# Kernel tuning notes

Measured on AMD Instinct MI355X. Metric: run time of the kernel, lower is better.

The kernel has to match this reference:

```python
import jax, jax.numpy as jnp
import numpy as np

TOP_K = 2


def setup_inputs() -> dict:
    key = jax.random.key(0)
    k0, k1, k2, k3, k4 = jax.random.split(key, 5)
    B, S, H, F, E = 2, 1024, 2048, 7168, 8
    scale = 0.02
    return {
        "hidden_states": jax.random.normal(k0, (B, S, H), jnp.float32),
        "Wg": jax.random.normal(k1, (E, H), jnp.float32) * scale,
        "w1": jax.random.normal(k2, (E, F, H), jnp.float32) * scale,
        "w3": jax.random.normal(k3, (E, F, H), jnp.float32) * scale,
        "w2": jax.random.normal(k4, (E, H, F), jnp.float32) * scale,
    }


def reference(hidden_states, Wg, w1, w3, w2):
    B, S, H = hidden_states.shape
    E = Wg.shape[0]
    x = hidden_states.reshape(-1, H)                      # [T, H]
    T = x.shape[0]

    # Router: logits -> softmax (float32) -> top-k -> renormalize
    router_logits = jnp.einsum("th,eh->te", x, Wg)        # [T, E]
    probs = jax.nn.softmax(router_logits.astype(jnp.float32), axis=-1)
    top_w, top_idx = jax.lax.top_k(probs, TOP_K)          # [T, K]
    top_w = top_w / jnp.sum(top_w, axis=-1, keepdims=True)
    top_w = top_w.astype(x.dtype)

    # Combine weights: [T, E], zero for unselected experts
    combine = jnp.zeros((T, E), x.dtype).at[
        jnp.arange(T)[:, None], top_idx
    ].add(top_w)

    out = jnp.zeros((T, H), x.dtype)
    for e in range(E):
        h = jax.nn.silu(x @ w1[e].T) * (x @ w3[e].T)      # [T, F]
        out = out + (h @ w2[e].T) * combine[:, e:e + 1]   # [T, H]

    return out.reshape(B, S, H), router_logits
```

## Files before the change

### kernel.cpp

```cpp
#include <hip/hip_runtime.h>

#define T_TOK 2048
#define H_DIM 2048
#define F_DIM 7168
#define E_NUM 8
#define MAX_SLOTS 5120
#define BM 128
#define BN 128
#define BK 64

typedef __attribute__((ext_vector_type(8))) _Float16 f16x8;
typedef __attribute__((ext_vector_type(4))) _Float16 f16x4;
typedef __attribute__((ext_vector_type(4))) float    f32x4;

#define GLL(g, l) __builtin_amdgcn_global_load_lds(                          \
    (const __attribute__((address_space(1))) void*)(g),                      \
    (__attribute__((address_space(3))) void*)(l), 16, 0, 0)


__global__ __launch_bounds__(256) void cvtw_kernel(const float* __restrict__ src,
                                                   _Float16* __restrict__ dst) {
    size_t i = ((size_t)blockIdx.x * 256 + threadIdx.x) * 8;
    float4 a = *(const float4*)(src + i);
    float4 b = *(const float4*)(src + i + 4);
    f16x8 h;
    h[0]=(_Float16)a.x; h[1]=(_Float16)a.y; h[2]=(_Float16)a.z; h[3]=(_Float16)a.w;
    h[4]=(_Float16)b.x; h[5]=(_Float16)b.y; h[6]=(_Float16)b.z; h[7]=(_Float16)b.w;
    *(f16x8*)(dst + i) = h;
}

__global__ __launch_bounds__(256) void router_kernel(
    const float* __restrict__ x, const float* __restrict__ wg,
    float* __restrict__ logits_out, int* __restrict__ tk_e,
    float* __restrict__ tk_w, int* __restrict__ meta) {
    int wave = threadIdx.x >> 6;
    int lane = threadIdx.x & 63;
    int t = blockIdx.x * 4 + wave;
    const float* xr = x + (size_t)t * H_DIM;

    float xv[32];
#pragma unroll
    for (int i = 0; i < 8; i++) {
        float4 v = *(const float4*)(xr + i * 256 + lane * 4);
        xv[i*4+0] = v.x; xv[i*4+1] = v.y; xv[i*4+2] = v.z; xv[i*4+3] = v.w;
    }
    float lg[E_NUM];
#pragma unroll
    for (int e = 0; e < E_NUM; e++) {
        const float* wr = wg + (size_t)e * H_DIM;
        float acc = 0.f;
#pragma unroll
        for (int i = 0; i < 8; i++) {
            float4 v = *(const float4*)(wr + i * 256 + lane * 4);
            acc += xv[i*4+0]*v.x + xv[i*4+1]*v.y + xv[i*4+2]*v.z + xv[i*4+3]*v.w;
        }
#pragma unroll
        for (int s = 32; s > 0; s >>= 1) acc += __shfl_xor(acc, s, 64);
        lg[e] = acc;
    }
    if (lane == 0) {
        float b0 = -3e38f, b1 = -3e38f; int i0 = 0, i1 = 0;
#pragma unroll
        for (int e = 0; e < E_NUM; e++) {
            float le = lg[e];
            if (le > b0)      { b1 = b0; i1 = i0; b0 = le; i0 = e; }
            else if (le > b1) { b1 = le; i1 = e; }
        }
        float w0 = 1.f / (1.f + __expf(b1 - b0));
        float w1v = 1.f - w0;
#pragma unroll
        for (int e = 0; e < E_NUM; e++) logits_out[(size_t)t * E_NUM + e] = lg[e];
        tk_e[t*2+0] = i0; tk_w[t*2+0] = w0;
        tk_e[t*2+1] = i1; tk_w[t*2+1] = w1v;
        atomicAdd(&meta[i0], 1);
        atomicAdd(&meta[i1], 1);
    }
}

__global__ void scan_kernel(int* __restrict__ meta, int* __restrict__ slot_tok,
                            float* __restrict__ slot_w) {
    int lane = threadIdx.x;
    int cnts[E_NUM], pads[E_NUM], bases[E_NUM];
    int run = 0;
#pragma unroll
    for (int e = 0; e < E_NUM; e++) {
        cnts[e] = meta[e];
        pads[e] = (cnts[e] + BM - 1) & ~(BM - 1);
        bases[e] = run;
        run += pads[e];
    }
    if (lane < E_NUM) { meta[8 + lane] = pads[lane]; meta[16 + lane] = bases[lane]; }
    for (int e = 0; e < E_NUM; e++)
        for (int i = cnts[e] + lane; i < pads[e]; i += 64) {
            slot_tok[bases[e] + i] = 0;
            slot_w[bases[e] + i] = 0.f;
        }
}

__global__ __launch_bounds__(256) void assign_kernel(
    const int* __restrict__ tk_e, const float* __restrict__ tk_w,
    int* __restrict__ meta, int* __restrict__ slot_tok, float* __restrict__ slot_w) {
    int t = blockIdx.x * 256 + threadIdx.x;
    if (t >= T_TOK) return;
#pragma unroll
    for (int k = 0; k < 2; k++) {
        int e = tk_e[t*2+k];
        int pos = atomicAdd(&meta[24 + e], 1);
        int s = meta[16 + e] + pos;
        slot_tok[s] = t;
        slot_w[s] = tk_w[t*2+k];
    }
}


__global__ __launch_bounds__(256, 2) void ffn1_kernel(
    const _Float16* __restrict__ xb, const _Float16* __restrict__ w1h,
    const _Float16* __restrict__ w3h, const int* __restrict__ slot_tok,
    const int* __restrict__ meta, _Float16* __restrict__ hbuf) {
    int e = blockIdx.z;
    int cntpad = meta[8 + e];
    int mb = blockIdx.y;
    if (mb * BM >= cntpad) return;
    int base = meta[16 + e];
    int nb = blockIdx.x;

    __shared__ _Float16 sA[BM][BK];
    __shared__ _Float16 sB1[BN][BK];
    __shared__ _Float16 sB3[BN][BK];

    int tid = threadIdx.x;
    int lane = tid & 63;
    int wave = tid >> 6;
    int wm = wave >> 1, wn = wave & 1;
    int lr = lane & 15, lk = (lane >> 4) * 8;

    int rsub = lane >> 3;
    int colc = (lane & 7) * 8;
    int slot0 = base + mb * BM;

    const _Float16* aG[4];
    const _Float16* b1G[4];
    const _Float16* b3G[4];
#pragma unroll
    for (int q = 0; q < 4; q++) {
        int row = wave * 32 + q * 8 + rsub;
        int tok = slot_tok[slot0 + row];
        aG[q] = xb + (size_t)tok * H_DIM + colc;
        size_t wrow = (size_t)e * F_DIM + (size_t)nb * BN + row;
        b1G[q] = w1h + wrow * H_DIM + colc;
        b3G[q] = w3h + wrow * H_DIM + colc;
    }

    f32x4 zero = {0.f, 0.f, 0.f, 0.f};
    f32x4 acc1[4][4], acc3[4][4];
#pragma unroll
    for (int m = 0; m < 4; m++)
#pragma unroll
        for (int n = 0; n < 4; n++) { acc1[m][n] = zero; acc3[m][n] = zero; }

    for (int k0 = 0; k0 < H_DIM; k0 += BK) {
        __syncthreads();
#pragma unroll
        for (int q = 0; q < 4; q++) {
            GLL(aG[q] + k0,  &sA[wave * 32 + q * 8][0]);
            GLL(b1G[q] + k0, &sB1[wave * 32 + q * 8][0]);
            GLL(b3G[q] + k0, &sB3[wave * 32 + q * 8][0]);
        }
        __syncthreads();
#pragma unroll
        for (int ks = 0; ks < BK; ks += 32) {
            f16x8 af[4], bf1[4], bf3[4];
#pragma unroll
            for (int m = 0; m < 4; m++)
                af[m] = *(const f16x8*)(const void*)&sA[wm*64 + m*16 + lr][ks + lk];
#pragma unroll
            for (int n = 0; n < 4; n++) {
                bf1[n] = *(const f16x8*)(const void*)&sB1[wn*64 + n*16 + lr][ks + lk];
                bf3[n] = *(const f16x8*)(const void*)&sB3[wn*64 + n*16 + lr][ks + lk];
            }
#pragma unroll
            for (int m = 0; m < 4; m++)
#pragma unroll
                for (int n = 0; n < 4; n++) {
                    acc1[m][n] = __builtin_amdgcn_mfma_f32_16x16x32_f16(af[m], bf1[n], acc1[m][n], 0, 0, 0);
                    acc3[m][n] = __builtin_amdgcn_mfma_f32_16x16x32_f16(af[m], bf3[n], acc3[m][n], 0, 0, 0);
                }
        }
    }
    int row0 = mb * BM + wm * 64;
    int col0 = nb * BN + wn * 64;
#pragma unroll
    for (int m = 0; m < 4; m++) {
#pragma unroll
        for (int n = 0; n < 4; n++) {
            int col = col0 + n * 16 + lr;
            f32x4 v1 = acc1[m][n], v3 = acc3[m][n];
#pragma unroll
            for (int j = 0; j < 4; j++) {
                int slot = base + row0 + m * 16 + (lane >> 4) * 4 + j;
                float a1 = v1[j], a3 = v3[j];
                float hv = a1 * a3 / (1.f + __expf(-a1));
                hbuf[(size_t)slot * F_DIM + col] = (_Float16)hv;
            }
        }
    }
}

__global__ __launch_bounds__(256, 2) void ffn2_kernel(
    const _Float16* __restrict__ hbuf, const _Float16* __restrict__ w2h,
    const int* __restrict__ slot_tok, const float* __restrict__ slot_w,
    const int* __restrict__ meta, float* __restrict__ out) {
    int e = blockIdx.z;
    int cntpad = meta[8 + e];
    int mb = blockIdx.y;
    if (mb * BM >= cntpad) return;
    int base = meta[16 + e];
    int nb = blockIdx.x;

    __shared__ _Float16 sA[BM][BK];
    __shared__ _Float16 sB[BN][BK];

    int tid = threadIdx.x;
    int lane = tid & 63;
    int wave = tid >> 6;
    int wm = wave >> 1, wn = wave & 1;
    int lr = lane & 15, lk = (lane >> 4) * 8;

    int rsub = lane >> 3;
    int colc = (lane & 7) * 8;
    int slot0 = base + mb * BM;

    const _Float16* aG[4];
    const _Float16* bG[4];
#pragma unroll
    for (int q = 0; q < 4; q++) {
        int row = wave * 32 + q * 8 + rsub;
        aG[q] = hbuf + (size_t)(slot0 + row) * F_DIM + colc;
        bG[q] = w2h + ((size_t)e * H_DIM + (size_t)nb * BN + row) * F_DIM + colc;
    }

    f32x4 zero = {0.f, 0.f, 0.f, 0.f};
    f32x4 acc[4][4];
#pragma unroll
    for (int m = 0; m < 4; m++)
#pragma unroll
        for (int n = 0; n < 4; n++) acc[m][n] = zero;

    for (int k0 = 0; k0 < F_DIM; k0 += BK) {
        __syncthreads();
#pragma unroll
        for (int q = 0; q < 4; q++) {
            GLL(aG[q] + k0, &sA[wave * 32 + q * 8][0]);
            GLL(bG[q] + k0, &sB[wave * 32 + q * 8][0]);
        }
        __syncthreads();
#pragma unroll
        for (int ks = 0; ks < BK; ks += 32) {
            f16x8 af[4], bf[4];
#pragma unroll
            for (int m = 0; m < 4; m++)
                af[m] = *(const f16x8*)(const void*)&sA[wm*64 + m*16 + lr][ks + lk];
#pragma unroll
            for (int n = 0; n < 4; n++)
                bf[n] = *(const f16x8*)(const void*)&sB[wn*64 + n*16 + lr][ks + lk];
#pragma unroll
            for (int m = 0; m < 4; m++)
#pragma unroll
                for (int n = 0; n < 4; n++)
                    acc[m][n] = __builtin_amdgcn_mfma_f32_16x16x32_f16(af[m], bf[n], acc[m][n], 0, 0, 0);
        }
    }
    int row0 = mb * BM + wm * 64;
    int col0 = nb * BN + wn * 64;
#pragma unroll
    for (int m = 0; m < 4; m++) {
        int rb = row0 + m * 16 + (lane >> 4) * 4;
        int toks[4]; float wts[4];
#pragma unroll
        for (int j = 0; j < 4; j++) {
            int s = base + rb + j;
            toks[j] = slot_tok[s];
            wts[j]  = slot_w[s];
        }
#pragma unroll
        for (int n = 0; n < 4; n++) {
            int col = col0 + n * 16 + lr;
            f32x4 v = acc[m][n];
#pragma unroll
            for (int j = 0; j < 4; j++)
                atomicAdd(&out[(size_t)toks[j] * H_DIM + col], v[j] * wts[j]);
        }
    }
}

extern "C" void kernel_launch(void* const* d_in, const int* in_sizes, int n_in,
                              void* d_out, int out_size, void* d_ws, size_t ws_size,
                              hipStream_t stream) {
    const float* x  = (const float*)d_in[0];
    const float* wg = (const float*)d_in[1];
    const float* w1 = (const float*)d_in[2];
    const float* w3 = (const float*)d_in[3];
    const float* w2 = (const float*)d_in[4];
    float* out = (float*)d_out;
    float* logits = out + (size_t)T_TOK * H_DIM;

    const size_t WELEM = (size_t)E_NUM * F_DIM * H_DIM;

    char* ws = (char*)d_ws;
    _Float16* w1h  = (_Float16*)ws;
    _Float16* w3h  = w1h + WELEM;
    _Float16* w2h  = w3h + WELEM;
    _Float16* hbuf = w2h + WELEM;
    _Float16* xb   = hbuf + (size_t)MAX_SLOTS * F_DIM;
    char* p = (char*)(xb + (size_t)T_TOK * H_DIM);
    int*   slot_tok = (int*)p;   p += MAX_SLOTS * 4;
    float* slot_w   = (float*)p; p += MAX_SLOTS * 4;
    int*   tk_e     = (int*)p;   p += T_TOK * 2 * 4;
    float* tk_w     = (float*)p; p += T_TOK * 2 * 4;
    int*   meta     = (int*)p;

    hipMemsetAsync(d_out, 0, (size_t)out_size * sizeof(float), stream);
    hipMemsetAsync(meta, 0, 32 * sizeof(int), stream);

    cvtw_kernel<<<dim3(WELEM / (256 * 8)), 256, 0, stream>>>(w1, w1h);
    cvtw_kernel<<<dim3(WELEM / (256 * 8)), 256, 0, stream>>>(w3, w3h);
    cvtw_kernel<<<dim3(WELEM / (256 * 8)), 256, 0, stream>>>(w2, w2h);
    cvtw_kernel<<<dim3((size_t)T_TOK * H_DIM / (256 * 8)), 256, 0, stream>>>(x, xb);

    router_kernel<<<dim3(T_TOK / 4), 256, 0, stream>>>(x, wg, logits, tk_e, tk_w, meta);
    scan_kernel<<<dim3(1), 64, 0, stream>>>(meta, slot_tok, slot_w);
    assign_kernel<<<dim3(T_TOK / 256), 256, 0, stream>>>(tk_e, tk_w, meta, slot_tok, slot_w);

    ffn1_kernel<<<dim3(F_DIM / BN, 16, E_NUM), 256, 0, stream>>>(xb, w1h, w3h, slot_tok, meta, hbuf);
    ffn2_kernel<<<dim3(H_DIM / BN, 16, E_NUM), 256, 0, stream>>>(hbuf, w2h, slot_tok, slot_w, meta, out);
}
```

Before: 1.147 ms.

## Interleave w1/w3 weights, enlarge tiles, double-buffer LDS with swizzle in FFN kernels

Converts w1 and w3 into one interleaved fp16 buffer in 32-row blocks, so ffn1 runs a single 256x256 GEMM tile with 512 threads and applies the SiLU gate by pairing accumulator columns. Both FFN kernels now double-buffer LDS with global_load_lds prefetch two tiles ahead, use explicit vmcnt waits and raw barriers, and XOR-swizzle the LDS layout to avoid bank conflicts. ffn2 also moves to 128x256 tiles with 8 waves. The aim is to hide global load latency and raise MFMA utilisation. The cost is higher register and LDS pressure, with a possible occupancy risk from the larger tiles.

```diff
diff --git a/kernel.cpp b/kernel.cpp
--- a/kernel.cpp
+++ b/kernel.cpp
@@ -5,18 +5,33 @@
 #define F_DIM 7168
 #define E_NUM 8
 #define MAX_SLOTS 5120
-#define BM 128
-#define BN 128
-#define BK 64
+#define N13 (2 * F_DIM)
 
 typedef __attribute__((ext_vector_type(8))) _Float16 f16x8;
-typedef __attribute__((ext_vector_type(4))) _Float16 f16x4;
 typedef __attribute__((ext_vector_type(4))) float    f32x4;
 
 #define GLL(g, l) __builtin_amdgcn_global_load_lds(                          \
     (const __attribute__((address_space(1))) void*)(g),                      \
     (__attribute__((address_space(3))) void*)(l), 16, 0, 0)
 
+
+__global__ __launch_bounds__(256) void cvt13_kernel(const float* __restrict__ w1,
+                                                    const float* __restrict__ w3,
+                                                    _Float16* __restrict__ w13h) {
+    int b = blockIdx.x;
+    int e = b / N13;
+    int c = b - e * N13;
+    int blk = c >> 6, sub = c & 63;
+    int f = blk * 32 + (sub & 31);
+    const float* src = (sub < 32 ? w1 : w3) + ((size_t)e * F_DIM + f) * H_DIM + threadIdx.x * 8;
+    _Float16* dst = w13h + (size_t)b * H_DIM + threadIdx.x * 8;
+    float4 a = *(const float4*)src;
+    float4 bb = *(const float4*)(src + 4);
+    f16x8 h;
+    h[0]=(_Float16)a.x;  h[1]=(_Float16)a.y;  h[2]=(_Float16)a.z;  h[3]=(_Float16)a.w;
+    h[4]=(_Float16)bb.x; h[5]=(_Float16)bb.y; h[6]=(_Float16)bb.z; h[7]=(_Float16)bb.w;
+    *(f16x8*)dst = h;
+}
 
 __global__ __launch_bounds__(256) void cvtw_kernel(const float* __restrict__ src,
                                                    _Float16* __restrict__ dst) {
@@ -29,6 +44,7 @@
     *(f16x8*)(dst + i) = h;
 }
 
+
 __global__ __launch_bounds__(256) void router_kernel(
     const float* __restrict__ x, const float* __restrict__ wg,
     float* __restrict__ logits_out, int* __restrict__ tk_e,
@@ -85,7 +101,7 @@
 #pragma unroll
     for (int e = 0; e < E_NUM; e++) {
         cnts[e] = meta[e];
-        pads[e] = (cnts[e] + BM - 1) & ~(BM - 1);
+        pads[e] = (cnts[e] + 127) & ~127;
         bases[e] = run;
         run += pads[e];
     }
@@ -112,132 +128,160 @@
     }
 }
 
-
-__global__ __launch_bounds__(256, 2) void ffn1_kernel(
-    const _Float16* __restrict__ xb, const _Float16* __restrict__ w1h,
-    const _Float16* __restrict__ w3h, const int* __restrict__ slot_tok,
-    const int* __restrict__ meta, _Float16* __restrict__ hbuf) {
+__global__ __launch_bounds__(512, 2) void ffn1_kernel(
+    const _Float16* __restrict__ xb, const _Float16* __restrict__ w13h,
+    const int* __restrict__ slot_tok, const int* __restrict__ meta,
+    _Float16* __restrict__ hbuf) {
     int e = blockIdx.z;
     int cntpad = meta[8 + e];
     int mb = blockIdx.y;
-    if (mb * BM >= cntpad) return;
+    if (mb * 256 >= cntpad) return;
     int base = meta[16 + e];
     int nb = blockIdx.x;
 
-    __shared__ _Float16 sA[BM][BK];
-    __shared__ _Float16 sB1[BN][BK];
-    __shared__ _Float16 sB3[BN][BK];
-
-    int tid = threadIdx.x;
+    __shared__ _Float16 sA[2][256][64];
+    __shared__ _Float16 sB[2][256][64];
+
+    int tid  = threadIdx.x;
     int lane = tid & 63;
     int wave = tid >> 6;
-    int wm = wave >> 1, wn = wave & 1;
-    int lr = lane & 15, lk = (lane >> 4) * 8;
+    int wm = wave >> 2, wn = wave & 3;
+    int w8 = wave * 8;
+
+    int lr = lane & 15;
+    int sw = lane & 7;
+    int sg = lane >> 4;
+    int offk0 = lr * 64 + ((sg    ) ^ sw) * 8;
+    int offk1 = lr * 64 + ((sg + 4) ^ sw) * 8;
 
     int rsub = lane >> 3;
-    int colc = (lane & 7) * 8;
-    int slot0 = base + mb * BM;
+    int sl   = (lane & 7) ^ rsub;
+    int slot0 = base + mb * 256;
 
     const _Float16* aG[4];
-    const _Float16* b1G[4];
-    const _Float16* b3G[4];
+    const _Float16* bG[4];
 #pragma unroll
     for (int q = 0; q < 4; q++) {
-        int row = wave * 32 + q * 8 + rsub;
-        int tok = slot_tok[slot0 + row];
-        aG[q] = xb + (size_t)tok * H_DIM + colc;
-        size_t wrow = (size_t)e * F_DIM + (size_t)nb * BN + row;
-        b1G[q] = w1h + wrow * H_DIM + colc;
-        b3G[q] = w3h + wrow * H_DIM + colc;
+        int r = mb * 256 + q * 64 + w8 + rsub;
+        int tok = (r < cntpad) ? slot_tok[base + r] : 0;
+        aG[q] = xb + (size_t)tok * H_DIM + sl * 8;
+        bG[q] = w13h + ((size_t)e * N13 + (size_t)nb * 256 + q * 64 + w8 + rsub) * H_DIM + sl * 8;
     }
 
     f32x4 zero = {0.f, 0.f, 0.f, 0.f};
-    f32x4 acc1[4][4], acc3[4][4];
-#pragma unroll
-    for (int m = 0; m < 4; m++)
-#pragma unroll
-        for (int n = 0; n < 4; n++) { acc1[m][n] = zero; acc3[m][n] = zero; }
-
-    for (int k0 = 0; k0 < H_DIM; k0 += BK) {
-        __syncthreads();
-#pragma unroll
-        for (int q = 0; q < 4; q++) {
-            GLL(aG[q] + k0,  &sA[wave * 32 + q * 8][0]);
-            GLL(b1G[q] + k0, &sB1[wave * 32 + q * 8][0]);
-            GLL(b3G[q] + k0, &sB3[wave * 32 + q * 8][0]);
-        }
-        __syncthreads();
-#pragma unroll
-        for (int ks = 0; ks < BK; ks += 32) {
-            f16x8 af[4], bf1[4], bf3[4];
-#pragma unroll
-            for (int m = 0; m < 4; m++)
-                af[m] = *(const f16x8*)(const void*)&sA[wm*64 + m*16 + lr][ks + lk];
+    f32x4 acc[8][4];
+#pragma unroll
+    for (int m = 0; m < 8; m++)
+#pragma unroll
+        for (int n = 0; n < 4; n++) acc[m][n] = zero;
+
+    const int NT = H_DIM / 64;
+#pragma unroll
+    for (int q = 0; q < 4; q++) GLL(aG[q] + 0,  &sA[0][q*64 + w8][0]);
+#pragma unroll
+    for (int q = 0; q < 4; q++) GLL(bG[q] + 0,  &sB[0][q*64 + w8][0]);
+#pragma unroll
+    for (int q = 0; q < 4; q++) GLL(aG[q] + 64, &sA[1][q*64 + w8][0]);
+#pragma unroll
+    for (int q = 0; q < 4; q++) GLL(bG[q] + 64, &sB[1][q*64 + w8][0]);
+
+    for (int t = 0; t < NT; ++t) {
+        if (t < NT - 1) asm volatile("s_waitcnt vmcnt(8)" ::: "memory");
+        else            asm volatile("s_waitcnt vmcnt(0)" ::: "memory");
+        __builtin_amdgcn_sched_barrier(0);
+        __builtin_amdgcn_s_barrier();
+        __builtin_amdgcn_sched_barrier(0);
+        int bd = t & 1;
+        const _Float16* Ab = &sA[bd][wm * 128][0];
+        const _Float16* Bb = &sB[bd][wn * 64][0];
+        f16x8 bf[2][4];
+#pragma unroll
+        for (int n = 0; n < 4; n++) {
+            bf[0][n] = *(const f16x8*)(const void*)(Bb + n * 1024 + offk0);
+            bf[1][n] = *(const f16x8*)(const void*)(Bb + n * 1024 + offk1);
+        }
+        __builtin_amdgcn_s_setprio(1);
+#pragma unroll
+        for (int m = 0; m < 8; m++) {
+            f16x8 a0 = *(const f16x8*)(const void*)(Ab + m * 1024 + offk0);
+            f16x8 a1 = *(const f16x8*)(const void*)(Ab + m * 1024 + offk1);
 #pragma unroll
             for (int n = 0; n < 4; n++) {
-                bf1[n] = *(const f16x8*)(const void*)&sB1[wn*64 + n*16 + lr][ks + lk];
-                bf3[n] = *(const f16x8*)(const void*)&sB3[wn*64 + n*16 + lr][ks + lk];
+                acc[m][n] = __builtin_amdgcn_mfma_f32_16x16x32_f16(a0, bf[0][n], acc[m][n], 0, 0, 0);
+                acc[m][n] = __builtin_amdgcn_mfma_f32_16x16x32_f16(a1, bf[1][n], acc[m][n], 0, 0, 0);
             }
-#pragma unroll
-            for (int m = 0; m < 4; m++)
-#pragma unroll
-                for (int n = 0; n < 4; n++) {
-                    acc1[m][n] = __builtin_amdgcn_mfma_f32_16x16x32_f16(af[m], bf1[n], acc1[m][n], 0, 0, 0);
-                    acc3[m][n] = __builtin_amdgcn_mfma_f32_16x16x32_f16(af[m], bf3[n], acc3[m][n], 0, 0, 0);
+        }
+        __builtin_amdgcn_s_setprio(0);
+        __builtin_amdgcn_sched_barrier(0);
+        __builtin_amdgcn_s_barrier();
+        __builtin_amdgcn_sched_barrier(0);
+        if (t + 2 < NT) {
+            int k2 = (t + 2) * 64;
+#pragma unroll
+            for (int q = 0; q < 4; q++) GLL(aG[q] + k2, &sA[bd][q*64 + w8][0]);
+#pragma unroll
+            for (int q = 0; q < 4; q++) GLL(bG[q] + k2, &sB[bd][q*64 + w8][0]);
+        }
+    }
+
+    int row_e0 = mb * 256 + wm * 128;
+    int fb = nb * 128 + wn * 32;
+#pragma unroll
+    for (int m = 0; m < 8; m++) {
+#pragma unroll
+        for (int j = 0; j < 4; j++) {
+            int re = row_e0 + m * 16 + (lane >> 4) * 4 + j;
+            if (re < cntpad) {
+                size_t srow = (size_t)(base + re) * F_DIM;
+#pragma unroll
+                for (int n = 0; n < 2; n++) {
+                    float a1 = acc[m][n][j], a3 = acc[m][n + 2][j];
+                    float hv = a1 * a3 / (1.f + __expf(-a1));
+                    hbuf[srow + fb + n * 16 + lr] = (_Float16)hv;
                 }
-        }
-    }
-    int row0 = mb * BM + wm * 64;
-    int col0 = nb * BN + wn * 64;
-#pragma unroll
-    for (int m = 0; m < 4; m++) {
-#pragma unroll
-        for (int n = 0; n < 4; n++) {
-            int col = col0 + n * 16 + lr;
-            f32x4 v1 = acc1[m][n], v3 = acc3[m][n];
-#pragma unroll
-            for (int j = 0; j < 4; j++) {
-                int slot = base + row0 + m * 16 + (lane >> 4) * 4 + j;
-                float a1 = v1[j], a3 = v3[j];
-                float hv = a1 * a3 / (1.f + __expf(-a1));
-                hbuf[(size_t)slot * F_DIM + col] = (_Float16)hv;
             }
         }
     }
 }
 
-__global__ __launch_bounds__(256, 2) void ffn2_kernel(
+__global__ __launch_bounds__(512, 2) void ffn2_kernel(
     const _Float16* __restrict__ hbuf, const _Float16* __restrict__ w2h,
     const int* __restrict__ slot_tok, const float* __restrict__ slot_w,
     const int* __restrict__ meta, float* __restrict__ out) {
     int e = blockIdx.z;
     int cntpad = meta[8 + e];
     int mb = blockIdx.y;
-    if (mb * BM >= cntpad) return;
+    if (mb * 128 >= cntpad) return;
     int base = meta[16 + e];
     int nb = blockIdx.x;
 
-    __shared__ _Float16 sA[BM][BK];
-    __shared__ _Float16 sB[BN][BK];
-
-    int tid = threadIdx.x;
+    __shared__ _Float16 sA[2][128][64];
+    __shared__ _Float16 sB[2][256][64];
+
+    int tid  = threadIdx.x;
     int lane = tid & 63;
     int wave = tid >> 6;
-    int wm = wave >> 1, wn = wave & 1;
-    int lr = lane & 15, lk = (lane >> 4) * 8;
+    int wm = wave >> 2, wn = wave & 3;
+    int w8 = wave * 8;
+
+    int lr = lane & 15;
+    int sw = lane & 7;
+    int sg = lane >> 4;
+    int offk0 = lr * 64 + ((sg    ) ^ sw) * 8;
+    int offk1 = lr * 64 + ((sg + 4) ^ sw) * 8;
 
     int rsub = lane >> 3;
-    int colc = (lane & 7) * 8;
-    int slot0 = base + mb * BM;
-
-    const _Float16* aG[4];
+    int sl   = (lane & 7) ^ rsub;
+    int slot0 = base + mb * 128;
+
+    const _Float16* aG[2];
     const _Float16* bG[4];
 #pragma unroll
-    for (int q = 0; q < 4; q++) {
-        int row = wave * 32 + q * 8 + rsub;
-        aG[q] = hbuf + (size_t)(slot0 + row) * F_DIM + colc;
-        bG[q] = w2h + ((size_t)e * H_DIM + (size_t)nb * BN + row) * F_DIM + colc;
-    }
+    for (int q = 0; q < 2; q++)
+        aG[q] = hbuf + (size_t)(slot0 + q * 64 + w8 + rsub) * F_DIM + sl * 8;
+#pragma unroll
+    for (int q = 0; q < 4; q++)
+        bG[q] = w2h + ((size_t)e * H_DIM + (size_t)nb * 256 + q * 64 + w8 + rsub) * F_DIM + sl * 8;
 
     f32x4 zero = {0.f, 0.f, 0.f, 0.f};
     f32x4 acc[4][4];
@@ -246,32 +290,57 @@
 #pragma unroll
         for (int n = 0; n < 4; n++) acc[m][n] = zero;
 
-    for (int k0 = 0; k0 < F_DIM; k0 += BK) {
-        __syncthreads();
-#pragma unroll
-        for (int q = 0; q < 4; q++) {
-            GLL(aG[q] + k0, &sA[wave * 32 + q * 8][0]);
-            GLL(bG[q] + k0, &sB[wave * 32 + q * 8][0]);
-        }
-        __syncthreads();
-#pragma unroll
-        for (int ks = 0; ks < BK; ks += 32) {
-            f16x8 af[4], bf[4];
-#pragma unroll
-            for (int m = 0; m < 4; m++)
-                af[m] = *(const f16x8*)(const void*)&sA[wm*64 + m*16 + lr][ks + lk];
-#pragma unroll
-            for (int n = 0; n < 4; n++)
-                bf[n] = *(const f16x8*)(const void*)&sB[wn*64 + n*16 + lr][ks + lk];
-#pragma unroll
-            for (int m = 0; m < 4; m++)
-#pragma unroll
-                for (int n = 0; n < 4; n++)
-                    acc[m][n] = __builtin_amdgcn_mfma_f32_16x16x32_f16(af[m], bf[n], acc[m][n], 0, 0, 0);
-        }
-    }
-    int row0 = mb * BM + wm * 64;
-    int col0 = nb * BN + wn * 64;
+    const int NT = F_DIM / 64;
+#pragma unroll
+    for (int q = 0; q < 2; q++) GLL(aG[q] + 0,  &sA[0][q*64 + w8][0]);
+#pragma unroll
+    for (int q = 0; q < 4; q++) GLL(bG[q] + 0,  &sB[0][q*64 + w8][0]);
+#pragma unroll
+    for (int q = 0; q < 2; q++) GLL(aG[q] + 64, &sA[1][q*64 + w8][0]);
+#pragma unroll
+    for (int q = 0; q < 4; q++) GLL(bG[q] + 64, &sB[1][q*64 + w8][0]);
+
+    for (int t = 0; t < NT; ++t) {
+        if (t < NT - 1) asm volatile("s_waitcnt vmcnt(6)" ::: "memory");
+        else            asm volatile("s_waitcnt vmcnt(0)" ::: "memory");
+        __builtin_amdgcn_sched_barrier(0);
+        __builtin_amdgcn_s_barrier();
+        __builtin_amdgcn_sched_barrier(0);
+        int bd = t & 1;
+        const _Float16* Ab = &sA[bd][wm * 64][0];
+        const _Float16* Bb = &sB[bd][wn * 64][0];
+        f16x8 bf[2][4];
+#pragma unroll
+        for (int n = 0; n < 4; n++) {
+            bf[0][n] = *(const f16x8*)(const void*)(Bb + n * 1024 + offk0);
+            bf[1][n] = *(const f16x8*)(const void*)(Bb + n * 1024 + offk1);
+        }
+        __builtin_amdgcn_s_setprio(1);
+#pragma unroll
+        for (int m = 0; m < 4; m++) {
+            f16x8 a0 = *(const f16x8*)(const void*)(Ab + m * 1024 + offk0);
+            f16x8 a1 = *(const f16x8*)(const void*)(Ab + m * 1024 + offk1);
+#pragma unroll
+            for (int n = 0; n < 4; n++) {
+                acc[m][n] = __builtin_amdgcn_mfma_f32_16x16x32_f16(a0, bf[0][n], acc[m][n], 0, 0, 0);
+                acc[m][n] = __builtin_amdgcn_mfma_f32_16x16x32_f16(a1, bf[1][n], acc[m][n], 0, 0, 0);
+            }
+        }
+        __builtin_amdgcn_s_setprio(0);
+        __builtin_amdgcn_sched_barrier(0);
+        __builtin_amdgcn_s_barrier();
+        __builtin_amdgcn_sched_barrier(0);
+        if (t + 2 < NT) {
+            int k2 = (t + 2) * 64;
+#pragma unroll
+            for (int q = 0; q < 2; q++) GLL(aG[q] + k2, &sA[bd][q*64 + w8][0]);
+#pragma unroll
+            for (int q = 0; q < 4; q++) GLL(bG[q] + k2, &sB[bd][q*64 + w8][0]);
+        }
+    }
+
+    int row0 = mb * 128 + wm * 64;
+    int col0 = nb * 256 + wn * 64;
 #pragma unroll
     for (int m = 0; m < 4; m++) {
         int rb = row0 + m * 16 + (lane >> 4) * 4;
@@ -307,9 +376,8 @@
     const size_t WELEM = (size_t)E_NUM * F_DIM * H_DIM;
 
     char* ws = (char*)d_ws;
-    _Float16* w1h  = (_Float16*)ws;
-    _Float16* w3h  = w1h + WELEM;
-    _Float16* w2h  = w3h + WELEM;
+    _Float16* w13h = (_Float16*)ws;
+    _Float16* w2h  = w13h + 2 * WELEM;
     _Float16* hbuf = w2h + WELEM;
     _Float16* xb   = hbuf + (size_t)MAX_SLOTS * F_DIM;
     char* p = (char*)(xb + (size_t)T_TOK * H_DIM);
@@ -322,8 +390,7 @@
     hipMemsetAsync(d_out, 0, (size_t)out_size * sizeof(float), stream);
     hipMemsetAsync(meta, 0, 32 * sizeof(int), stream);
 
-    cvtw_kernel<<<dim3(WELEM / (256 * 8)), 256, 0, stream>>>(w1, w1h);
-    cvtw_kernel<<<dim3(WELEM / (256 * 8)), 256, 0, stream>>>(w3, w3h);
+    cvt13_kernel<<<dim3(E_NUM * N13), 256, 0, stream>>>(w1, w3, w13h);
     cvtw_kernel<<<dim3(WELEM / (256 * 8)), 256, 0, stream>>>(w2, w2h);
     cvtw_kernel<<<dim3((size_t)T_TOK * H_DIM / (256 * 8)), 256, 0, stream>>>(x, xb);
 
@@ -331,6 +398,6 @@
     scan_kernel<<<dim3(1), 64, 0, stream>>>(meta, slot_tok, slot_w);
     assign_kernel<<<dim3(T_TOK / 256), 256, 0, stream>>>(tk_e, tk_w, meta, slot_tok, slot_w);
 
-    ffn1_kernel<<<dim3(F_DIM / BN, 16, E_NUM), 256, 0, stream>>>(xb, w1h, w3h, slot_tok, meta, hbuf);
-    ffn2_kernel<<<dim3(H_DIM / BN, 16, E_NUM), 256, 0, stream>>>(hbuf, w2h, slot_tok, slot_w, meta, out);
-}
+    ffn1_kernel<<<dim3(N13 / 256, 8, E_NUM), 512, 0, stream>>>(xb, w13h, slot_tok, meta, hbuf);
+    ffn2_kernel<<<dim3(H_DIM / 256, 16, E_NUM), 512, 0, stream>>>(hbuf, w2h, slot_tok, slot_w, meta, out);
+}
```

New measurement: 1.292 ms. 12.6% more time.
